# Kernel optimization log

Hardware: AMD Instinct MI355X
Metric: run time of the kernel (lower is better)

The kernel has to match this reference:

```python
import jax, jax.numpy as jnp
import numpy as np

SIGMA = 1e-4   # SoftRas coverage sharpness
GAMMA = 0.1    # depth-softmax temperature
IMAGE_SIZE = 128


def _normalize(v):
    return v / (jnp.linalg.norm(v, axis=-1, keepdims=True) + 1e-8)


def _look_at(eye, center, up):
    z = _normalize(eye - center)
    x = _normalize(jnp.cross(up, z))
    y = jnp.cross(z, x)
    R = jnp.stack([x, y, z], axis=-2)                       # (B,3,3)
    t = -jnp.einsum('bij,bj->bi', R, eye)
    B = eye.shape[0]
    M = jnp.tile(jnp.eye(4, dtype=eye.dtype), (B, 1, 1))
    M = M.at[:, :3, :3].set(R).at[:, :3, 3].set(t)
    return M


def _perspective(fov_y, aspect, near, far):
    f = 1.0 / np.tan(fov_y / 2.0)
    M = np.zeros((4, 4), np.float32)
    M[0, 0] = f / aspect
    M[1, 1] = f
    M[2, 2] = (far + near) / (near - far)
    M[2, 3] = 2.0 * far * near / (near - far)
    M[3, 2] = -1.0
    return jnp.asarray(M)


def _project(verts_world, eye, center, up):
    B, V, _ = verts_world.shape
    view = _look_at(eye, center, up)
    proj = _perspective(np.deg2rad(60.0), 1.0, 0.1, 10.0)
    M = jnp.einsum('ij,bjk->bik', proj, view)
    vh = jnp.concatenate([verts_world, jnp.ones((B, V, 1), verts_world.dtype)], -1)
    clip = jnp.einsum('bij,bvj->bvi', M, vh)
    return clip[..., :3] / (clip[..., 3:4] + 1e-8)            # (B,V,3) NDC


def _edge_dist(p, a, b):
    # p: (H,W,2); a,b: (B,F,2) -> unsigned point-to-segment distance (B,F,H,W)
    pa = p[None, None] - a[:, :, None, None]                  # (B,F,H,W,2)
    ba = (b - a)[:, :, None, None]                            # (B,F,1,1,2)
    t = jnp.clip(jnp.sum(pa * ba, -1) / (jnp.sum(ba * ba, -1) + 1e-12), 0.0, 1.0)
    d = pa - t[..., None] * ba
    return jnp.sqrt(jnp.sum(d * d, -1) + 1e-12)


def _cross2(u, v):
    return u[..., 0] * v[..., 1] - u[..., 1] * v[..., 0]


def _rasterize(verts_ndc, faces, colors, image_size):
    tri = verts_ndc[:, faces]                                 # (B,F,3,3)
    v2, vz = tri[..., :2], tri[..., 2]                        # (B,F,3,2), (B,F,3)
    xs = (jnp.arange(image_size) + 0.5) / image_size * 2.0 - 1.0
    ys = 1.0 - (jnp.arange(image_size) + 0.5) / image_size * 2.0
    X, Y = jnp.meshgrid(xs, ys, indexing='xy')
    p = jnp.stack([X, Y], -1)                                 # (H,W,2)

    a0, a1, a2 = v2[:, :, 0], v2[:, :, 1], v2[:, :, 2]        # (B,F,2)
    area = _cross2(a1 - a0, a2 - a0)[:, :, None, None]        # (B,F,1,1)
    denom = area + jnp.where(area >= 0, 1e-12, -1e-12)
    w0 = _cross2((a2 - a1)[:, :, None, None], p[None, None] - a1[:, :, None, None])
    w1 = _cross2((a0 - a2)[:, :, None, None], p[None, None] - a2[:, :, None, None])
    w2 = _cross2((a1 - a0)[:, :, None, None], p[None, None] - a0[:, :, None, None])
    b0, b1, b2 = w0 / denom, w1 / denom, w2 / denom           # barycentrics (B,F,H,W)
    inside = (b0 >= 0) & (b1 >= 0) & (b2 >= 0)

    d = jnp.minimum(jnp.minimum(_edge_dist(p, a0, a1), _edge_dist(p, a1, a2)),
                    _edge_dist(p, a2, a0))
    sgn = jnp.where(inside, 1.0, -1.0)
    prob = jax.nn.sigmoid(sgn * d * d / SIGMA)                # soft coverage (B,F,H,W)
    sil = 1.0 - jnp.prod(1.0 - prob, axis=1, keepdims=True)   # (B,1,H,W)

    bc0, bc1, bc2 = (jnp.clip(b0, 0., 1.), jnp.clip(b1, 0., 1.), jnp.clip(b2, 0., 1.))
    s = bc0 + bc1 + bc2 + 1e-8
    zpix = (bc0 * vz[:, :, 0, None, None] + bc1 * vz[:, :, 1, None, None]
            + bc2 * vz[:, :, 2, None, None]) / s
    zn = jnp.clip((1.0 - zpix) * 0.5, 0.0, 1.0)               # 1 = near
    m = jnp.max(zn, axis=1, keepdims=True)
    Dw = prob * jnp.exp((zn - m) / GAMMA)
    w_bg = jnp.exp((0.0 - m) / GAMMA)                         # background (far, black)
    Wn = Dw / (jnp.sum(Dw, axis=1, keepdims=True) + w_bg)     # (B,F,H,W)
    face_col = jnp.mean(colors[:, faces], axis=2)             # (B,F,3)
    rgb = jnp.einsum('bfhw,bfc->bchw', Wn, face_col)          # (B,3,H,W)
    return sil, rgb


def setup_inputs() -> dict:
    key = jax.random.key(0)
    k1, k2, k3, k4 = jax.random.split(key, 4)
    B, V, F = 4, 256, 256
    verts_world = jax.random.normal(k1, (B, V, 3), jnp.float32) * 0.5
    faces = jax.random.randint(k2, (F, 3), 0, V)
    colors = jax.random.uniform(k3, (B, V, 3), jnp.float32)
    eye = jnp.tile(jnp.array([0.0, 0.0, 2.5], jnp.float32), (B, 1)) \
          + jax.random.normal(k4, (B, 3), jnp.float32) * 0.05
    return {"verts_world": verts_world, "faces": faces, "colors": colors, "eye": eye}


def reference(verts_world, faces, colors, eye):
    B = verts_world.shape[0]
    center = jnp.zeros((B, 3), verts_world.dtype)
    up = jnp.tile(jnp.array([0.0, 1.0, 0.0], verts_world.dtype), (B, 1))
    verts_ndc = _project(verts_world, eye, center, up)
    return _rasterize(verts_ndc, faces, colors, IMAGE_SIZE)
```

## Files before the change

kernel.cpp:

```cpp
#include <hip/hip_runtime.h>

#define NB 4
#define NV 256
#define NF 256
#define IMG 128
#define STRIDE 64

typedef float v2f __attribute__((ext_vector_type(2)));

__device__ __forceinline__ float rcpf(float x) { return __builtin_amdgcn_rcpf(x); }
__device__ __forceinline__ float ex2(float x)  { return __builtin_amdgcn_exp2f(x); }
__device__ __forceinline__ float med01(float x) { return __builtin_amdgcn_fmed3f(x, 0.0f, 1.0f); }
__device__ __forceinline__ v2f med01_2(v2f v) { return (v2f){ med01(v.x), med01(v.y) }; }
__device__ __forceinline__ v2f fma2(v2f a, v2f b, v2f c) { return __builtin_elementwise_fma(a, b, c); }


__global__ void prep_faces(const float* __restrict__ verts,
                           const int* __restrict__ faces,
                           const float* __restrict__ colors,
                           const float* __restrict__ eye,
                           float* __restrict__ fd)
{
    int gid = blockIdx.x * blockDim.x + threadIdx.x;
    if (gid >= NB * NF) return;
    int b = gid >> 8;
    int f = gid & 255;

    const float fpj = 1.7320508075688772f;
    const float p22 = -1.0202020202020203f;
    const float p23 = -0.20202020202020202f;
    const float SC  = 120.11224139682566f;
    const float ISC = 1.0f / 120.11224139682566f;

    float ex = eye[b*3+0], ey = eye[b*3+1], ez = eye[b*3+2];
    float en  = sqrtf(ex*ex + ey*ey + ez*ez);
    float izn = 1.0f / (en + 1e-8f);
    float zx = ex*izn, zy = ey*izn, zz = ez*izn;
    float cn  = sqrtf(zz*zz + zx*zx);
    float ixn = 1.0f / (cn + 1e-8f);
    float xx = zz*ixn, xy = 0.0f, xz = -zx*ixn;
    float yx = zy*xz - zz*xy;
    float yy = zz*xx - zx*xz;
    float yz = zx*xy - zy*xx;
    float tx = -(xx*ex + xy*ey + xz*ez);
    float ty = -(yx*ex + yy*ey + yz*ez);
    float tz = -(zx*ex + zy*ey + zz*ez);

    int i0 = faces[f*3+0], i1 = faces[f*3+1], i2 = faces[f*3+2];
    int idx[3] = { i0, i1, i2 };

    float ax[3], ay[3], az[3];
#pragma unroll
    for (int k = 0; k < 3; ++k) {
        const float* v = verts + (b*NV + idx[k])*3;
        float vx = v[0], vy = v[1], vz = v[2];
        float cx  = fpj*(xx*vx + xy*vy + xz*vz + tx);
        float cyv = fpj*(yx*vx + yy*vy + yz*vz + ty);
        float zv  = zx*vx + zy*vy + zz*vz + tz;
        float cz  = p22*zv + p23;
        float cw  = -zv;
        float iw  = 1.0f / (cw + 1e-8f);
        ax[k] = cx*iw; ay[k] = cyv*iw; az[k] = cz*iw;
    }

    float a0x = ax[0], a0y = ay[0];
    float a1x = ax[1], a1y = ay[1];
    float a2x = ax[2], a2y = ay[2];

    float e01x = a1x - a0x, e01y = a1y - a0y;
    float e12x = a2x - a1x, e12y = a2y - a1y;
    float e20x = a0x - a2x, e20y = a0y - a2y;

    float area  = e01x*(a2y - a0y) - e01y*(a2x - a0x);
    float denom = area + (area >= 0.0f ? 1e-12f : -1e-12f);
    float idn   = 1.0f / denom;

    float A0 = -e12y*idn, B0 = e12x*idn, C0 = (e12y*a1x - e12x*a1y)*idn;
    float A1 = -e20y*idn, B1 = e20x*idn, C1 = (e20y*a2x - e20x*a2y)*idn;
    float A2 = -e01y*idn, B2 = e01x*idn, C2 = (e01y*a0x - e01x*a0y)*idn;

    float ib01 = 1.0f / (e01x*e01x + e01y*e01y + 1e-12f);
    float ib12 = 1.0f / (e12x*e12x + e12y*e12y + 1e-12f);
    float ib20 = 1.0f / (e20x*e20x + e20y*e20y + 1e-12f);

    const float third = (1.0f/3.0f);
    float cr = (colors[(b*NV+i0)*3+0] + colors[(b*NV+i1)*3+0] + colors[(b*NV+i2)*3+0]) * third;
    float cg = (colors[(b*NV+i0)*3+1] + colors[(b*NV+i1)*3+1] + colors[(b*NV+i2)*3+1]) * third;
    float cb = (colors[(b*NV+i0)*3+2] + colors[(b*NV+i1)*3+2] + colors[(b*NV+i2)*3+2]) * third;

    float* o = fd + (b*128 + (f >> 1))*STRIDE + (f & 1);
    o[ 0]=A0;   o[ 2]=B0;   o[ 4]=C0;
    o[ 6]=A1;   o[ 8]=B1;   o[10]=C1;
    o[12]=A2;   o[14]=B2;   o[16]=C2;
    o[18]=a0x*SC;  o[20]=a0y*SC;
    o[22]=e01x*SC; o[24]=e01y*SC; o[26]=e12x*SC; o[28]=e12y*SC; o[30]=e20x*SC; o[32]=e20y*SC;
    o[34]=e01x*ib01*ISC; o[36]=e01y*ib01*ISC;
    o[38]=e12x*ib12*ISC; o[40]=e12y*ib12*ISC;
    o[42]=e20x*ib20*ISC; o[44]=e20y*ib20*ISC;
    o[46]=az[0]; o[48]=az[1]; o[50]=az[2];
    o[52]=cr;   o[54]=cg;   o[56]=cb;
    o[58]=0.0f; o[60]=0.0f; o[62]=0.0f;
}

__launch_bounds__(512)
__global__ void raster(const float* __restrict__ fd, float* __restrict__ out)
{
    __shared__ float sFD[8192];

    const int t   = threadIdx.x;
    const int cy  = threadIdx.y;
    const int b   = blockIdx.x >> 8;
    const int grp = blockIdx.x & 255;
    const int pixb = grp*64 + t;
    const int h = pixb >> 7;
    const int w = pixb & 127;

    {
        const float4* src = (const float4*)(fd + (b << 13));
        float4* dst = (float4*)sFD;
        int tid = (cy << 6) + t;
#pragma unroll
        for (int k = 0; k < 4; ++k) dst[tid + (k << 9)] = src[tid + (k << 9)];
    }
    __syncthreads();

    const float px = (w + 0.5f) * (1.0f/64.0f) - 1.0f;
    const float py = 1.0f - (h + 0.5f) * (1.0f/64.0f);
    const float SC = 120.11224139682566f;
    const v2f px2  = { px, px };
    const v2f py2  = { py, py };
    const v2f pxs2 = { px*SC, px*SC };
    const v2f pys2 = { py*SC, py*SC };

    const float KGAM = 14.426950408889634f;
    const v2f KGH_NEG = { -0.5f*KGAM, -0.5f*KGAM };
    const v2f KGH_POS = {  0.5f*KGAM,  0.5f*KGAM };
    const v2f ONE2 = { 1.0f, 1.0f };
    const v2f EPS2 = { 1e-8f, 1e-8f };

    const float* fc = sFD + cy*(16*STRIDE);

    v2f prod2 = { 1.0f, 1.0f };
    v2f S2  = { 0.0f, 0.0f };
    v2f R02 = { 0.0f, 0.0f };
    v2f R12 = { 0.0f, 0.0f };
    v2f R22 = { 0.0f, 0.0f };

#pragma unroll 2
    for (int i = 0; i < 16; ++i) {
        const float* c = fc + i*STRIDE;
#define LD(k) (*(const v2f*)(c + 2*(k)))
        v2f A0 = LD(0),  B0 = LD(1),  C0 = LD(2);
        v2f A1 = LD(3),  B1 = LD(4),  C1 = LD(5);
        v2f A2 = LD(6),  B2 = LD(7),  C2 = LD(8);
        v2f a0x = LD(9), a0y = LD(10);
        v2f e01x = LD(11), e01y = LD(12);
        v2f e12x = LD(13), e12y = LD(14);
        v2f e20x = LD(15), e20y = LD(16);
        v2f g01x = LD(17), g01y = LD(18);
        v2f g12x = LD(19), g12y = LD(20);
        v2f g20x = LD(21), g20y = LD(22);
        v2f z0 = LD(23), z1 = LD(24), z2 = LD(25);
        v2f cr = LD(26), cg = LD(27), cb = LD(28);
#undef LD

        v2f b0 = fma2(A0, px2, fma2(B0, py2, C0));
        v2f b1 = fma2(A1, px2, fma2(B1, py2, C1));
        v2f b2 = fma2(A2, px2, fma2(B2, py2, C2));

        v2f pa0x = pxs2 - a0x, pa0y = pys2 - a0y;
        v2f pa1x = pa0x - e01x, pa1y = pa0y - e01y;
        v2f pa2x = pa0x + e20x, pa2y = pa0y + e20y;

        v2f tt = med01_2(fma2(pa0x, g01x, pa0y*g01y));
        v2f dx = fma2(-tt, e01x, pa0x);
        v2f dy = fma2(-tt, e01y, pa0y);
        v2f dd0 = fma2(dx, dx, dy*dy);
        tt = med01_2(fma2(pa1x, g12x, pa1y*g12y));
        dx = fma2(-tt, e12x, pa1x);
        dy = fma2(-tt, e12y, pa1y);
        v2f dd1 = fma2(dx, dx, dy*dy);
        tt = med01_2(fma2(pa2x, g20x, pa2y*g20y));
        dx = fma2(-tt, e20x, pa2x);
        dy = fma2(-tt, e20y, pa2y);
        v2f dd2 = fma2(dx, dx, dy*dy);

        float ddl = fminf(fminf(dd0.x, dd1.x), dd2.x);
        float ddh = fminf(fminf(dd0.y, dd1.y), dd2.y);
        float mxl = fmaxf(fmaxf(-b0.x, -b1.x), -b2.x);
        float mxh = fmaxf(fmaxf(-b0.y, -b1.y), -b2.y);
        float qx = copysignf(ddl, mxl);
        float qy = copysignf(ddh, mxh);

        v2f e2  = { ex2(qx), ex2(qy) };
        v2f den = e2 + ONE2;
        v2f prob = { rcpf(den.x), rcpf(den.y) };

        prod2 = fma2(-prob, prod2, prod2);

        v2f bc0 = med01_2(b0), bc1 = med01_2(b1), bc2 = med01_2(b2);
        v2f s   = (bc0 + bc1) + (bc2 + EPS2);
        v2f zs  = fma2(bc0, z0, fma2(bc1, z1, bc2*z2));
        v2f irs = { rcpf(s.x), rcpf(s.y) };
        v2f zq  = fma2(zs*irs, KGH_NEG, KGH_POS);
        float znx = __builtin_amdgcn_fmed3f(zq.x, 0.0f, KGAM);
        float zny = __builtin_amdgcn_fmed3f(zq.y, 0.0f, KGAM);
        v2f ez  = { ex2(znx), ex2(zny) };
        v2f wgt = prob * ez;

        S2  = S2 + wgt;
        R02 = fma2(wgt, cr, R02);
        R12 = fma2(wgt, cg, R12);
        R22 = fma2(wgt, cb, R22);
    }

    __syncthreads();
    float* red = sFD;
    red[(0*8 + cy)*64 + t] = prod2.x * prod2.y;
    red[(1*8 + cy)*64 + t] = S2.x  + S2.y;
    red[(2*8 + cy)*64 + t] = R02.x + R02.y;
    red[(3*8 + cy)*64 + t] = R12.x + R12.y;
    red[(4*8 + cy)*64 + t] = R22.x + R22.y;
    __syncthreads();

    if (cy == 0) {
        float P  = 1.0f, St = 0.0f, r0 = 0.0f, r1 = 0.0f, r2 = 0.0f;
#pragma unroll
        for (int c2 = 0; c2 < 8; ++c2) {
            P  *= red[(0*8 + c2)*64 + t];
            St += red[(1*8 + c2)*64 + t];
            r0 += red[(2*8 + c2)*64 + t];
            r1 += red[(3*8 + c2)*64 + t];
            r2 += red[(4*8 + c2)*64 + t];
        }
        float iden = rcpf(St + 1.0f);

        out[b*16384 + pixb] = 1.0f - P;
        float* rgb = out + 65536;
        rgb[(b*3 + 0)*16384 + pixb] = r0 * iden;
        rgb[(b*3 + 1)*16384 + pixb] = r1 * iden;
        rgb[(b*3 + 2)*16384 + pixb] = r2 * iden;
    }
}

extern "C" void kernel_launch(void* const* d_in, const int* in_sizes, int n_in,
                              void* d_out, int out_size, void* d_ws, size_t ws_size,
                              hipStream_t stream)
{
    const float* verts  = (const float*)d_in[0];
    const int*   faces  = (const int*)d_in[1];
    const float* colors = (const float*)d_in[2];
    const float* eye    = (const float*)d_in[3];
    float* out = (float*)d_out;
    float* fd  = (float*)d_ws;

    hipLaunchKernelGGL(prep_faces, dim3(4), dim3(256), 0, stream,
                       verts, faces, colors, eye, fd);
    hipLaunchKernelGGL(raster, dim3(1024), dim3(64, 8), 0, stream, fd, out);
}
```

Before: 34.87 us.

## Bin face pairs into 8x8 pixel tiles and skip non-overlapping faces

The prep kernel now computes a screen-space bounding box per face, padded by a small margin, and builds a per-tile list of face pairs whose boxes overlap each 8x8 pixel tile. The raster kernel switches from 64-pixel rows to 8x8 tiles and walks only the listed face pairs, spread across the 8 thread rows. The per-face record is halved: barycentric coefficients, the third edge and the inverse edge lengths are rebuilt in the loop from fewer stored values, cutting the shared-memory staging. Culling relies on coverage beyond the margin being negligible at this sigma. Per-tile lists can be uneven across thread rows, and the binning pass runs serially over 128 pairs per thread.

```diff
diff --git a/kernel.cpp b/kernel.cpp
--- a/kernel.cpp
+++ b/kernel.cpp
@@ -4,7 +4,7 @@
 #define NV 256
 #define NF 256
 #define IMG 128
-#define STRIDE 64
+#define STR 32
 
 typedef float v2f __attribute__((ext_vector_type(2)));
 
@@ -13,24 +13,27 @@
 __device__ __forceinline__ float med01(float x) { return __builtin_amdgcn_fmed3f(x, 0.0f, 1.0f); }
 __device__ __forceinline__ v2f med01_2(v2f v) { return (v2f){ med01(v.x), med01(v.y) }; }
 __device__ __forceinline__ v2f fma2(v2f a, v2f b, v2f c) { return __builtin_elementwise_fma(a, b, c); }
+__device__ __forceinline__ int rfl(int x) { return __builtin_amdgcn_readfirstlane(x); }
+
+#define SCV   120.11224139682566f
+#define ISC2  6.931471805599453e-05f
+#define KGAMV 14.426950408889634f
 
 
 __global__ void prep_faces(const float* __restrict__ verts,
                            const int* __restrict__ faces,
                            const float* __restrict__ colors,
                            const float* __restrict__ eye,
-                           float* __restrict__ fd)
+                           float* __restrict__ ws)
 {
-    int gid = blockIdx.x * blockDim.x + threadIdx.x;
-    if (gid >= NB * NF) return;
-    int b = gid >> 8;
-    int f = gid & 255;
+    __shared__ float4 sBB[256];
+
+    const int b = blockIdx.x;
+    const int f = threadIdx.x;
 
     const float fpj = 1.7320508075688772f;
     const float p22 = -1.0202020202020203f;
     const float p23 = -0.20202020202020202f;
-    const float SC  = 120.11224139682566f;
-    const float ISC = 1.0f / 120.11224139682566f;
 
     float ex = eye[b*3+0], ey = eye[b*3+1], ez = eye[b*3+2];
     float en  = sqrtf(ex*ex + ey*ey + ez*ez);
@@ -75,10 +78,6 @@
     float denom = area + (area >= 0.0f ? 1e-12f : -1e-12f);
     float idn   = 1.0f / denom;
 
-    float A0 = -e12y*idn, B0 = e12x*idn, C0 = (e12y*a1x - e12x*a1y)*idn;
-    float A1 = -e20y*idn, B1 = e20x*idn, C1 = (e20y*a2x - e20x*a2y)*idn;
-    float A2 = -e01y*idn, B2 = e01x*idn, C2 = (e01y*a0x - e01x*a0y)*idn;
-
     float ib01 = 1.0f / (e01x*e01x + e01y*e01y + 1e-12f);
     float ib12 = 1.0f / (e12x*e12x + e12y*e12y + 1e-12f);
     float ib20 = 1.0f / (e20x*e20x + e20y*e20y + 1e-12f);
@@ -88,143 +87,160 @@
     float cg = (colors[(b*NV+i0)*3+1] + colors[(b*NV+i1)*3+1] + colors[(b*NV+i2)*3+1]) * third;
     float cb = (colors[(b*NV+i0)*3+2] + colors[(b*NV+i1)*3+2] + colors[(b*NV+i2)*3+2]) * third;
 
-    float* o = fd + (b*128 + (f >> 1))*STRIDE + (f & 1);
-    o[ 0]=A0;   o[ 2]=B0;   o[ 4]=C0;
-    o[ 6]=A1;   o[ 8]=B1;   o[10]=C1;
-    o[12]=A2;   o[14]=B2;   o[16]=C2;
-    o[18]=a0x*SC;  o[20]=a0y*SC;
-    o[22]=e01x*SC; o[24]=e01y*SC; o[26]=e12x*SC; o[28]=e12y*SC; o[30]=e20x*SC; o[32]=e20y*SC;
-    o[34]=e01x*ib01*ISC; o[36]=e01y*ib01*ISC;
-    o[38]=e12x*ib12*ISC; o[40]=e12y*ib12*ISC;
-    o[42]=e20x*ib20*ISC; o[44]=e20y*ib20*ISC;
-    o[46]=az[0]; o[48]=az[1]; o[50]=az[2];
-    o[52]=cr;   o[54]=cg;   o[56]=cb;
-    o[58]=0.0f; o[60]=0.0f; o[62]=0.0f;
+    float* o = ws + (b*128 + (f >> 1))*STR + (f & 1);
+    o[ 0]=a0x*SCV;   o[ 2]=a0y*SCV;
+    o[ 4]=e01x*SCV;  o[ 6]=e01y*SCV;
+    o[ 8]=e12x*SCV;  o[10]=e12y*SCV;
+    o[12]=ib01*ISC2; o[14]=ib12*ISC2; o[16]=ib20*ISC2;
+    o[18]=idn*ISC2;
+    o[20]=az[0]; o[22]=az[1]; o[24]=az[2];
+    o[26]=cr;   o[28]=cg;   o[30]=cb;
+
+    float xmn = fminf(fminf(a0x, a1x), a2x);
+    float xmx = fmaxf(fmaxf(a0x, a1x), a2x);
+    float ymn = fminf(fminf(a0y, a1y), a2y);
+    float ymx = fmaxf(fmaxf(a0y, a1y), a2y);
+    sBB[f] = make_float4((xmn + 0.9375f)*64.0f - 0.5f,
+                         (xmx + 1.0625f)*64.0f - 0.5f,
+                         (0.9375f - ymx)*64.0f - 0.5f,
+                         (1.0625f - ymn)*64.0f - 0.5f);
+    __syncthreads();
+
+    {
+        const int tile = f;
+        const float tX0 = (float)((tile & 15) << 3);
+        const float tY0 = (float)((tile >> 4) << 3);
+        const float tX1 = tX0 + 7.0f;
+        const float tY1 = tY0 + 7.0f;
+        int* L = (int*)(ws + 16384) + ((b << 8) + tile)*132;
+        int cnt = 0;
+        for (int p = 0; p < 128; ++p) {
+            float4 b1 = sBB[2*p], b2 = sBB[2*p+1];
+            bool h1 = (b1.x <= tX1) && (b1.y >= tX0) && (b1.z <= tY1) && (b1.w >= tY0);
+            bool h2 = (b2.x <= tX1) && (b2.y >= tX0) && (b2.z <= tY1) && (b2.w >= tY0);
+            if (h1 || h2) L[1 + cnt++] = p;
+        }
+        L[0] = cnt;
+    }
 }
 
 __launch_bounds__(512)
-__global__ void raster(const float* __restrict__ fd, float* __restrict__ out)
+__global__ void raster(const float* __restrict__ ws, float* __restrict__ out)
 {
-    __shared__ float sFD[8192];
+    __shared__ float sFD[4096];
 
     const int t   = threadIdx.x;
     const int cy  = threadIdx.y;
-    const int b   = blockIdx.x >> 8;
-    const int grp = blockIdx.x & 255;
-    const int pixb = grp*64 + t;
-    const int h = pixb >> 7;
-    const int w = pixb & 127;
+    const int bid = blockIdx.x;
+    const int b    = bid >> 8;
+    const int tile = bid & 255;
+    const int tx0 = (tile & 15) << 3;
+    const int ty0 = (tile >> 4) << 3;
 
     {
-        const float4* src = (const float4*)(fd + (b << 13));
+        const float4* src = (const float4*)(ws + (b << 12));
         float4* dst = (float4*)sFD;
         int tid = (cy << 6) + t;
-#pragma unroll
-        for (int k = 0; k < 4; ++k) dst[tid + (k << 9)] = src[tid + (k << 9)];
-    }
-    __syncthreads();
-
-    const float px = (w + 0.5f) * (1.0f/64.0f) - 1.0f;
-    const float py = 1.0f - (h + 0.5f) * (1.0f/64.0f);
-    const float SC = 120.11224139682566f;
-    const v2f px2  = { px, px };
-    const v2f py2  = { py, py };
-    const v2f pxs2 = { px*SC, px*SC };
-    const v2f pys2 = { py*SC, py*SC };
-
-    const float KGAM = 14.426950408889634f;
-    const v2f KGH_NEG = { -0.5f*KGAM, -0.5f*KGAM };
-    const v2f KGH_POS = {  0.5f*KGAM,  0.5f*KGAM };
+        dst[tid]       = src[tid];
+        dst[tid + 512] = src[tid + 512];
+    }
+    __syncthreads();
+
+    const int w = tx0 + (t & 7);
+    const int h = ty0 + (t >> 3);
+    const float xs = ((w + 0.5f) * (1.0f/64.0f) - 1.0f) * SCV;
+    const float ys = (1.0f - (h + 0.5f) * (1.0f/64.0f)) * SCV;
+    const v2f PX = { xs, xs }, PY = { ys, ys };
+
+    const v2f KGH_NEG = { -0.5f*KGAMV, -0.5f*KGAMV };
+    const v2f KGH_POS = {  0.5f*KGAMV,  0.5f*KGAMV };
     const v2f ONE2 = { 1.0f, 1.0f };
     const v2f EPS2 = { 1e-8f, 1e-8f };
 
-    const float* fc = sFD + cy*(16*STRIDE);
-
-    v2f prod2 = { 1.0f, 1.0f };
-    v2f S2  = { 0.0f, 0.0f };
-    v2f R02 = { 0.0f, 0.0f };
-    v2f R12 = { 0.0f, 0.0f };
-    v2f R22 = { 0.0f, 0.0f };
-
-#pragma unroll 2
-    for (int i = 0; i < 16; ++i) {
-        const float* c = fc + i*STRIDE;
-#define LD(k) (*(const v2f*)(c + 2*(k)))
-        v2f A0 = LD(0),  B0 = LD(1),  C0 = LD(2);
-        v2f A1 = LD(3),  B1 = LD(4),  C1 = LD(5);
-        v2f A2 = LD(6),  B2 = LD(7),  C2 = LD(8);
-        v2f a0x = LD(9), a0y = LD(10);
-        v2f e01x = LD(11), e01y = LD(12);
-        v2f e12x = LD(13), e12y = LD(14);
-        v2f e20x = LD(15), e20y = LD(16);
-        v2f g01x = LD(17), g01y = LD(18);
-        v2f g12x = LD(19), g12y = LD(20);
-        v2f g20x = LD(21), g20y = LD(22);
-        v2f z0 = LD(23), z1 = LD(24), z2 = LD(25);
-        v2f cr = LD(26), cg = LD(27), cb = LD(28);
+    const int* L = (const int*)(ws + 16384) + bid*132;
+    const int cnt = rfl(L[0]);
+
+    v2f aP = ONE2, aS = {0,0}, aR0 = {0,0}, aR1 = {0,0}, aR2 = {0,0};
+
+    int k = cy;
+    int p = (k < cnt) ? rfl(L[1 + k]) : 0;
+    while (k < cnt) {
+        const int kn = k + 8;
+        const int pn = (kn < cnt) ? rfl(L[1 + kn]) : 0;
+
+        const float* c = sFD + p*STR;
+#define LD(q) (*(const v2f*)(c + 2*(q)))
+        v2f a0x = LD(0), a0y = LD(1);
+        v2f e01x = LD(2), e01y = LD(3);
+        v2f e12x = LD(4), e12y = LD(5);
+        v2f ib01 = LD(6), ib12 = LD(7), ib20 = LD(8);
+        v2f idn = LD(9);
+        v2f z0 = LD(10), z1 = LD(11), z2 = LD(12);
+        v2f cr = LD(13), cg = LD(14), cb = LD(15);
 #undef LD
-
-        v2f b0 = fma2(A0, px2, fma2(B0, py2, C0));
-        v2f b1 = fma2(A1, px2, fma2(B1, py2, C1));
-        v2f b2 = fma2(A2, px2, fma2(B2, py2, C2));
-
-        v2f pa0x = pxs2 - a0x, pa0y = pys2 - a0y;
+        v2f e20x = -(e01x + e12x), e20y = -(e01y + e12y);
+        v2f g01x = e01x*ib01, g01y = e01y*ib01;
+        v2f g12x = e12x*ib12, g12y = e12y*ib12;
+        v2f g20x = e20x*ib20, g20y = e20y*ib20;
+
+        v2f pa0x = PX - a0x, pa0y = PY - a0y;
         v2f pa1x = pa0x - e01x, pa1y = pa0y - e01y;
         v2f pa2x = pa0x + e20x, pa2y = pa0y + e20y;
+        v2f b0 = fma2(-e12y, pa1x, e12x*pa1y) * idn;
+        v2f b1 = fma2(-e20y, pa2x, e20x*pa2y) * idn;
+        v2f b2 = fma2(-e01y, pa0x, e01x*pa0y) * idn;
 
         v2f tt = med01_2(fma2(pa0x, g01x, pa0y*g01y));
         v2f dx = fma2(-tt, e01x, pa0x);
         v2f dy = fma2(-tt, e01y, pa0y);
-        v2f dd0 = fma2(dx, dx, dy*dy);
+        v2f ddA = fma2(dx, dx, dy*dy);
         tt = med01_2(fma2(pa1x, g12x, pa1y*g12y));
         dx = fma2(-tt, e12x, pa1x);
         dy = fma2(-tt, e12y, pa1y);
-        v2f dd1 = fma2(dx, dx, dy*dy);
+        v2f ddB = fma2(dx, dx, dy*dy);
         tt = med01_2(fma2(pa2x, g20x, pa2y*g20y));
         dx = fma2(-tt, e20x, pa2x);
         dy = fma2(-tt, e20y, pa2y);
-        v2f dd2 = fma2(dx, dx, dy*dy);
-
-        float ddl = fminf(fminf(dd0.x, dd1.x), dd2.x);
-        float ddh = fminf(fminf(dd0.y, dd1.y), dd2.y);
+        v2f ddC = fma2(dx, dx, dy*dy);
+
+        float ddl = fminf(fminf(ddA.x, ddB.x), ddC.x);
+        float ddh = fminf(fminf(ddA.y, ddB.y), ddC.y);
         float mxl = fmaxf(fmaxf(-b0.x, -b1.x), -b2.x);
         float mxh = fmaxf(fmaxf(-b0.y, -b1.y), -b2.y);
-        float qx = copysignf(ddl, mxl);
-        float qy = copysignf(ddh, mxh);
-
-        v2f e2  = { ex2(qx), ex2(qy) };
+        v2f q = { copysignf(ddl, mxl), copysignf(ddh, mxh) };
+
+        v2f e2 = { ex2(q.x), ex2(q.y) };
         v2f den = e2 + ONE2;
         v2f prob = { rcpf(den.x), rcpf(den.y) };
-
-        prod2 = fma2(-prob, prod2, prod2);
+        aP = fma2(-prob, aP, aP);
 
         v2f bc0 = med01_2(b0), bc1 = med01_2(b1), bc2 = med01_2(b2);
-        v2f s   = (bc0 + bc1) + (bc2 + EPS2);
-        v2f zs  = fma2(bc0, z0, fma2(bc1, z1, bc2*z2));
+        v2f s = (bc0 + bc1) + (bc2 + EPS2);
+        v2f zs = fma2(bc0, z0, fma2(bc1, z1, bc2*z2));
         v2f irs = { rcpf(s.x), rcpf(s.y) };
-        v2f zq  = fma2(zs*irs, KGH_NEG, KGH_POS);
-        float znx = __builtin_amdgcn_fmed3f(zq.x, 0.0f, KGAM);
-        float zny = __builtin_amdgcn_fmed3f(zq.y, 0.0f, KGAM);
-        v2f ez  = { ex2(znx), ex2(zny) };
+        v2f zq = fma2(zs*irs, KGH_NEG, KGH_POS);
+        v2f ez = { ex2(__builtin_amdgcn_fmed3f(zq.x, 0.0f, KGAMV)),
+                   ex2(__builtin_amdgcn_fmed3f(zq.y, 0.0f, KGAMV)) };
         v2f wgt = prob * ez;
-
-        S2  = S2 + wgt;
-        R02 = fma2(wgt, cr, R02);
-        R12 = fma2(wgt, cg, R12);
-        R22 = fma2(wgt, cb, R22);
+        aS = aS + wgt;
+        aR0 = fma2(wgt, cr, aR0);
+        aR1 = fma2(wgt, cg, aR1);
+        aR2 = fma2(wgt, cb, aR2);
+
+        k = kn; p = pn;
     }
 
     __syncthreads();
     float* red = sFD;
-    red[(0*8 + cy)*64 + t] = prod2.x * prod2.y;
-    red[(1*8 + cy)*64 + t] = S2.x  + S2.y;
-    red[(2*8 + cy)*64 + t] = R02.x + R02.y;
-    red[(3*8 + cy)*64 + t] = R12.x + R12.y;
-    red[(4*8 + cy)*64 + t] = R22.x + R22.y;
+    red[(0*8 + cy)*64 + t] = aP.x * aP.y;
+    red[(1*8 + cy)*64 + t] = aS.x + aS.y;
+    red[(2*8 + cy)*64 + t] = aR0.x + aR0.y;
+    red[(3*8 + cy)*64 + t] = aR1.x + aR1.y;
+    red[(4*8 + cy)*64 + t] = aR2.x + aR2.y;
     __syncthreads();
 
     if (cy == 0) {
-        float P  = 1.0f, St = 0.0f, r0 = 0.0f, r1 = 0.0f, r2 = 0.0f;
+        float P = 1.0f, St = 0.0f, r0 = 0.0f, r1 = 0.0f, r2 = 0.0f;
 #pragma unroll
         for (int c2 = 0; c2 < 8; ++c2) {
             P  *= red[(0*8 + c2)*64 + t];
@@ -235,11 +251,12 @@
         }
         float iden = rcpf(St + 1.0f);
 
-        out[b*16384 + pixb] = 1.0f - P;
+        const int pix = h*IMG + w;
+        out[b*16384 + pix] = 1.0f - P;
         float* rgb = out + 65536;
-        rgb[(b*3 + 0)*16384 + pixb] = r0 * iden;
-        rgb[(b*3 + 1)*16384 + pixb] = r1 * iden;
-        rgb[(b*3 + 2)*16384 + pixb] = r2 * iden;
+        rgb[(b*3 + 0)*16384 + pix] = r0 * iden;
+        rgb[(b*3 + 1)*16384 + pix] = r1 * iden;
+        rgb[(b*3 + 2)*16384 + pix] = r2 * iden;
     }
 }
 
@@ -252,9 +269,9 @@
     const float* colors = (const float*)d_in[2];
     const float* eye    = (const float*)d_in[3];
     float* out = (float*)d_out;
-    float* fd  = (float*)d_ws;
-
-    hipLaunchKernelGGL(prep_faces, dim3(4), dim3(256), 0, stream,
-                       verts, faces, colors, eye, fd);
-    hipLaunchKernelGGL(raster, dim3(1024), dim3(64, 8), 0, stream, fd, out);
+    float* ws  = (float*)d_ws;
+
+    hipLaunchKernelGGL(prep_faces, dim3(4),    dim3(256), 0, stream,
+                       verts, faces, colors, eye, ws);
+    hipLaunchKernelGGL(raster,     dim3(1024), dim3(64, 8), 0, stream, ws, out);
 }
```

New measurement: 53.14 us. 52.4% more time.
